# Performance work log

Measured on AMD Instinct MI355X. Metric: run time of the kernel, lower is better.

## Reference

```python
import jax, jax.numpy as jnp
import numpy as np

TEMPERATURE = 2.0
SOFT_LAMBDA = 0.5
SMOOTH_L1_BETA = 1.0  # CFG.smooth_l1_beta (torch default)
EPS_COS = 1e-8
EPS_LOG = 1e-7


def _offdiag(x):
    # x: [n, n] -> [n, n-1], dropping the diagonal, preserving column order.
    n = x.shape[0]
    cols = jnp.arange(n - 1)
    idx = cols[None, :] + (cols[None, :] >= jnp.arange(n)[:, None])
    return x[jnp.arange(n)[:, None], idx]


def _cos_pair_diff(v):
    # 1 - pairwise cosine similarity, norms clamped at eps (torch CosineSimilarity).
    nv = jnp.maximum(jnp.linalg.norm(v, axis=-1), EPS_COS)
    cos = (v @ v.T) / (nv[:, None] * nv[None, :])
    return 1.0 - cos


def setup_inputs() -> dict:
    key = jax.random.key(0)
    k1, k2, k3, k4, k5 = jax.random.split(key, 5)
    n, d_feat = 384, 128
    return {
        "trans_feat": jax.random.normal(k1, (n, d_feat), dtype=jnp.float32),
        "rot_green": jax.random.normal(k2, (n, 3), dtype=jnp.float32),
        "rot_red": jax.random.normal(k3, (n, 3), dtype=jnp.float32),
        "trans": jax.random.normal(k4, (n, 3), dtype=jnp.float32),
        "sym": jax.random.randint(k5, (n, 1), 0, 2, dtype=jnp.int32),
    }


def reference(trans_feat, rot_green, rot_red, trans, sym):
    n = trans_feat.shape[0]

    # ---- label differences ----
    # trans: smooth-L1 over pairwise diffs, mean over coord dim -> [n, n]
    d = trans[:, None, :] - trans[None, :, :]
    ad = jnp.abs(d)
    sl1 = jnp.where(ad < SMOOTH_L1_BETA, 0.5 * d * d / SMOOTH_L1_BETA, ad - 0.5 * SMOOTH_L1_BETA)
    trans_diff = sl1.mean(-1)

    g = _cos_pair_diff(rot_green)
    r = _cos_pair_diff(rot_red)
    sym_mask = sym[:, 0] == 1
    pair_sym = sym_mask[:, None] | sym_mask[None, :]
    rot_diff = jnp.where(pair_sym, g, g + r)

    # ---- feature similarity logits (negative L2, zero-safe norm) ----
    fd = trans_feat[:, None, :] - trans_feat[None, :, :]
    sq = jnp.sum(fd * fd, axis=-1)
    norm = jnp.where(sq > 0, jnp.sqrt(jnp.where(sq > 0, sq, 1.0)), 0.0)
    logits = -norm / TEMPERATURE
    logits = logits - jnp.max(logits, axis=1, keepdims=True)
    exp_logits = jnp.exp(logits)

    lo = _offdiag(logits)      # [n, n-1]
    eo = _offdiag(exp_logits)  # [n, n-1]
    td = _offdiag(trans_diff)  # [n, n-1]
    rd = _offdiag(rot_diff)    # [n, n-1]

    # rank masks: mask[i, j, k] = diff[i, j] <= diff[i, k]
    trans_mask = td[:, :, None] <= td[:, None, :]
    hard_mask = trans_mask & (rd[:, :, None] <= rd[:, None, :])

    den_trans = jnp.einsum('ijk,ik->ij', trans_mask.astype(lo.dtype), eo)
    den_hard = jnp.einsum('ijk,ik->ij', hard_mask.astype(lo.dtype), eo)

    pos_trans = lo - jnp.log(den_trans + EPS_LOG)
    pos_hard = lo - jnp.log(den_hard + EPS_LOG)

    denom = n * (n - 1)
    loss_hard = -jnp.sum(pos_hard) / denom
    loss_trans = -jnp.sum(pos_trans) / denom
    return loss_hard + SOFT_LAMBDA * loss_trans
```

## Files before the change

kernel.cpp:

```cpp
#include <hip/hip_runtime.h>
#include <math.h>

#define N 384
#define HB 192
#define DF 128
#define TEMP 2.0f
#define SOFT_LAMBDA 0.5f
#define BETA 1.0f
#define EPS_COS 1e-8f
#define EPS_LOG 1e-7f

__global__ __launch_bounds__(192) void rnc_main(
    const float* __restrict__ feat,
    const float* __restrict__ rg,
    const float* __restrict__ rr,
    const float* __restrict__ tr,
    const int*   __restrict__ sym,
    float* __restrict__ partial_h,
    float* __restrict__ partial_t)
{
    const int i = blockIdx.x >> 1;
    const int h = blockIdx.x & 1;
    const int t = threadIdx.x;

    __shared__ __align__(16) float4 pk[N];
    __shared__ __align__(16) float2 dp[HB][4];
    __shared__ __align__(16) float fi[DF];
    __shared__ float hdr[12];
    __shared__ float red_h[3], red_t[3];

    if (t < DF) fi[t] = feat[i * DF + t];
    if (t == 0) {
        hdr[0] = tr[i * 3 + 0];
        hdr[1] = tr[i * 3 + 1];
        hdr[2] = tr[i * 3 + 2];
        float g0 = rg[i * 3 + 0], g1 = rg[i * 3 + 1], g2 = rg[i * 3 + 2];
        hdr[3] = g0; hdr[4] = g1; hdr[5] = g2;
        hdr[6] = fmaxf(sqrtf(g0 * g0 + g1 * g1 + g2 * g2), EPS_COS);
        float r0 = rr[i * 3 + 0], r1 = rr[i * 3 + 1], r2 = rr[i * 3 + 2];
        hdr[7] = r0; hdr[8] = r1; hdr[9] = r2;
        hdr[10] = fmaxf(sqrtf(r0 * r0 + r1 * r1 + r2 * r2), EPS_COS);
        hdr[11] = (sym[i] == 1) ? 1.0f : 0.0f;
    }
    __syncthreads();

    for (int e = t; e < N; e += HB) {
        const float4* fj4 = reinterpret_cast<const float4*>(feat + e * DF);
        const float4* fi4 = reinterpret_cast<const float4*>(fi);
        float sq = 0.f;
#pragma unroll 8
        for (int d = 0; d < DF / 4; ++d) {
            float4 a = fi4[d];
            float4 b = fj4[d];
            float dx = a.x - b.x, dy = a.y - b.y, dz = a.z - b.z, dw = a.w - b.w;
            sq += dx * dx + dy * dy + dz * dz + dw * dw;
        }
        float dist = (sq > 0.f) ? sqrtf(sq) : 0.f;
        float lo = -dist * (1.0f / TEMP);
        float eo = (e == i) ? 0.f : expf(lo);

        float s = 0.f;
#pragma unroll
        for (int c = 0; c < 3; ++c) {
            float d_ = hdr[c] - tr[e * 3 + c];
            float ad = fabsf(d_);
            s += (ad < BETA) ? (0.5f * d_ * d_ / BETA) : (ad - 0.5f * BETA);
        }
        float td = s * (1.0f / 3.0f);

        float g0 = rg[e * 3 + 0], g1 = rg[e * 3 + 1], g2 = rg[e * 3 + 2];
        float ng = fmaxf(sqrtf(g0 * g0 + g1 * g1 + g2 * g2), EPS_COS);
        float gdiff = 1.0f - (hdr[3] * g0 + hdr[4] * g1 + hdr[5] * g2) / (hdr[6] * ng);
        float r0 = rr[e * 3 + 0], r1 = rr[e * 3 + 1], r2 = rr[e * 3 + 2];
        float nr = fmaxf(sqrtf(r0 * r0 + r1 * r1 + r2 * r2), EPS_COS);
        float rdiff = 1.0f - (hdr[7] * r0 + hdr[8] * r1 + hdr[9] * r2) / (hdr[10] * nr);
        bool pair_sym = (hdr[11] != 0.0f) || (sym[e] == 1);
        float rd = pair_sym ? gdiff : (gdiff + rdiff);

        pk[e] = make_float4(td, rd, eo, lo);
    }
    __syncthreads();

    const int kg = t >> 6;
    const int l  = t & 63;
    const int jl = l * 3;
    float tdj[3], rdj[3];
    float dent[3] = {0.f, 0.f, 0.f};
    float denh[3] = {0.f, 0.f, 0.f};
#pragma unroll
    for (int jj = 0; jj < 3; ++jj) {
        float4 p = pk[h * HB + jl + jj];
        tdj[jj] = p.x;
        rdj[jj] = p.y;
    }
    const int k0 = kg * (N / 3);
#pragma unroll 4
    for (int k = k0; k < k0 + N / 3; ++k) {
        float4 p = pk[k];
#pragma unroll
        for (int jj = 0; jj < 3; ++jj) {
            bool mt = p.x >= tdj[jj];
            bool mh = mt && (p.y >= rdj[jj]);
            dent[jj] += mt ? p.z : 0.f;
            denh[jj] += mh ? p.z : 0.f;
        }
    }
#pragma unroll
    for (int jj = 0; jj < 3; ++jj) dp[jl + jj][kg] = make_float2(dent[jj], denh[jj]);
    __syncthreads();

    float st_ = 0.f, sh_ = 0.f;
#pragma unroll
    for (int g = 0; g < 3; ++g) {
        float2 v = dp[t][g];
        st_ += v.x;
        sh_ += v.y;
    }
    const int j = h * HB + t;
    float pos_h = 0.f, pos_t = 0.f;
    if (j != i) {
        float lo = pk[j].w;
        pos_h = lo - logf(sh_ + EPS_LOG);
        pos_t = lo - logf(st_ + EPS_LOG);
    }
#pragma unroll
    for (int off = 32; off > 0; off >>= 1) {
        pos_h += __shfl_down(pos_h, off, 64);
        pos_t += __shfl_down(pos_t, off, 64);
    }
    if (l == 0) {
        red_h[kg] = pos_h;
        red_t[kg] = pos_t;
    }
    __syncthreads();
    if (t == 0) {
        partial_h[blockIdx.x] = red_h[0] + red_h[1] + red_h[2];
        partial_t[blockIdx.x] = red_t[0] + red_t[1] + red_t[2];
    }
}

__global__ __launch_bounds__(768) void rnc_final(
    const float* __restrict__ partial_h,
    const float* __restrict__ partial_t,
    float* __restrict__ out)
{
    const int t = threadIdx.x;
    float hsum = partial_h[t];
    float tsum = partial_t[t];
#pragma unroll
    for (int off = 32; off > 0; off >>= 1) {
        hsum += __shfl_down(hsum, off, 64);
        tsum += __shfl_down(tsum, off, 64);
    }
    __shared__ float rh[12], rt[12];
    const int wave = t >> 6, lane = t & 63;
    if (lane == 0) {
        rh[wave] = hsum;
        rt[wave] = tsum;
    }
    __syncthreads();
    if (t == 0) {
        double sh = 0.0, st = 0.0;
#pragma unroll
        for (int w = 0; w < 12; ++w) {
            sh += (double)rh[w];
            st += (double)rt[w];
        }
        const double denom = (double)N * (double)(N - 1);
        out[0] = (float)(-(sh + (double)SOFT_LAMBDA * st) / denom);
    }
}

extern "C" void kernel_launch(void* const* d_in, const int* in_sizes, int n_in,
                              void* d_out, int out_size, void* d_ws, size_t ws_size,
                              hipStream_t stream) {
    const float* feat = (const float*)d_in[0];
    const float* rg   = (const float*)d_in[1];
    const float* rr   = (const float*)d_in[2];
    const float* tr   = (const float*)d_in[3];
    const int*   sym  = (const int*)d_in[4];
    float* out = (float*)d_out;

    float* partial_h = (float*)d_ws;
    float* partial_t = partial_h + 2 * N;

    rnc_main<<<2 * N, HB, 0, stream>>>(feat, rg, rr, tr, sym, partial_h, partial_t);
    rnc_final<<<1, 2 * N, 0, stream>>>(partial_h, partial_t, out);
}
```

Before: 93.45 us.

## Split pairwise feature computation into tiled kernel and widen rank kernel

Moves the pairwise distance, label-difference and exp computation into a separate 16x16-tiled kernel that stages both feature rows in shared memory and writes a full N×N float4 pair table to workspace. The rank kernel then loads one row of that table and uses 512 threads (8 k-groups) instead of 192, which shortens each thread's comparison loop. The aim is to avoid having every block re-read 384 feature rows from global memory, and to give the quadratic rank loop more parallelism. In exchange it adds an extra kernel launch, a 2.3 MB write and read-back of the pair table, and needs a larger workspace.

```diff
diff --git a/kernel.cpp b/kernel.cpp
--- a/kernel.cpp
+++ b/kernel.cpp
@@ -2,20 +2,98 @@
 #include <math.h>
 
 #define N 384
-#define HB 192
 #define DF 128
+#define TI 16
+#define TK 16
 #define TEMP 2.0f
 #define SOFT_LAMBDA 0.5f
 #define BETA 1.0f
 #define EPS_COS 1e-8f
 #define EPS_LOG 1e-7f
 
-__global__ __launch_bounds__(192) void rnc_main(
+__global__ __launch_bounds__(256) void rnc_pairs(
     const float* __restrict__ feat,
     const float* __restrict__ rg,
     const float* __restrict__ rr,
     const float* __restrict__ tr,
     const int*   __restrict__ sym,
+    float4* __restrict__ pk)
+{
+    const int i0 = blockIdx.y * TI;
+    const int k0 = blockIdx.x * TK;
+    const int t = threadIdx.x;
+
+    __shared__ __align__(16) float4 fi_s[TI][DF / 4 + 1];
+    __shared__ __align__(16) float4 fk_s[TK][DF / 4 + 1];
+    __shared__ float4 hi_s[TI], gi_s[TI], ri_s[TI];
+    __shared__ float4 hk_s[TK], gk_s[TK], rk_s[TK];
+
+    if (t < TI) {
+        int g = i0 + t;
+        hi_s[t] = make_float4(tr[g * 3], tr[g * 3 + 1], tr[g * 3 + 2],
+                              (sym[g] == 1) ? 1.f : 0.f);
+        float a = rg[g * 3], b = rg[g * 3 + 1], c = rg[g * 3 + 2];
+        gi_s[t] = make_float4(a, b, c, fmaxf(sqrtf(a * a + b * b + c * c), EPS_COS));
+        float d = rr[g * 3], e = rr[g * 3 + 1], f = rr[g * 3 + 2];
+        ri_s[t] = make_float4(d, e, f, fmaxf(sqrtf(d * d + e * e + f * f), EPS_COS));
+    } else if (t >= 32 && t < 32 + TK) {
+        int g = k0 + (t - 32);
+        int tl = t - 32;
+        hk_s[tl] = make_float4(tr[g * 3], tr[g * 3 + 1], tr[g * 3 + 2],
+                               (sym[g] == 1) ? 1.f : 0.f);
+        float a = rg[g * 3], b = rg[g * 3 + 1], c = rg[g * 3 + 2];
+        gk_s[tl] = make_float4(a, b, c, fmaxf(sqrtf(a * a + b * b + c * c), EPS_COS));
+        float d = rr[g * 3], e = rr[g * 3 + 1], f = rr[g * 3 + 2];
+        rk_s[tl] = make_float4(d, e, f, fmaxf(sqrtf(d * d + e * e + f * f), EPS_COS));
+    }
+
+    const float4* feat4 = reinterpret_cast<const float4*>(feat);
+#pragma unroll
+    for (int idx = 0; idx < 2; ++idx) {
+        int u = t + idx * 256;
+        int row = u >> 5, c = u & 31;
+        fi_s[row][c] = feat4[(i0 + row) * (DF / 4) + c];
+        fk_s[row][c] = feat4[(k0 + row) * (DF / 4) + c];
+    }
+    __syncthreads();
+
+    const int ii = t >> 4, kk = t & 15;
+    float sq = 0.f;
+#pragma unroll
+    for (int d = 0; d < DF / 4; ++d) {
+        float4 a = fi_s[ii][d];
+        float4 b = fk_s[kk][d];
+        float dx = a.x - b.x, dy = a.y - b.y, dz = a.z - b.z, dw = a.w - b.w;
+        sq += dx * dx + dy * dy + dz * dz + dw * dw;
+    }
+    const int gi = i0 + ii, gk = k0 + kk;
+    float dist = (sq > 0.f) ? sqrtf(sq) : 0.f;
+    float lo = -dist * (1.0f / TEMP);
+    float eo = (gi == gk) ? 0.f : expf(lo);
+
+    float4 ha = hi_s[ii], hb = hk_s[kk];
+    float s = 0.f;
+    {
+        float d0 = ha.x - hb.x, d1 = ha.y - hb.y, d2 = ha.z - hb.z;
+        float a0 = fabsf(d0), a1 = fabsf(d1), a2 = fabsf(d2);
+        s += (a0 < BETA) ? (0.5f * d0 * d0 / BETA) : (a0 - 0.5f * BETA);
+        s += (a1 < BETA) ? (0.5f * d1 * d1 / BETA) : (a1 - 0.5f * BETA);
+        s += (a2 < BETA) ? (0.5f * d2 * d2 / BETA) : (a2 - 0.5f * BETA);
+    }
+    float td = s * (1.0f / 3.0f);
+
+    float4 ga = gi_s[ii], gb = gk_s[kk];
+    float gdiff = 1.0f - (ga.x * gb.x + ga.y * gb.y + ga.z * gb.z) / (ga.w * gb.w);
+    float4 ra = ri_s[ii], rb = rk_s[kk];
+    float rdiff = 1.0f - (ra.x * rb.x + ra.y * rb.y + ra.z * rb.z) / (ra.w * rb.w);
+    bool pair_sym = (ha.w != 0.f) || (hb.w != 0.f);
+    float rd = pair_sym ? gdiff : (gdiff + rdiff);
+
+    pk[gi * N + gk] = make_float4(td, rd, eo, lo);
+}
+
+__global__ __launch_bounds__(512) void rnc_rank(
+    const float4* __restrict__ pk,
     float* __restrict__ partial_h,
     float* __restrict__ partial_t)
 {
@@ -23,80 +101,28 @@
     const int h = blockIdx.x & 1;
     const int t = threadIdx.x;
 
-    __shared__ __align__(16) float4 pk[N];
-    __shared__ __align__(16) float2 dp[HB][4];
-    __shared__ __align__(16) float fi[DF];
-    __shared__ float hdr[12];
-    __shared__ float red_h[3], red_t[3];
-
-    if (t < DF) fi[t] = feat[i * DF + t];
-    if (t == 0) {
-        hdr[0] = tr[i * 3 + 0];
-        hdr[1] = tr[i * 3 + 1];
-        hdr[2] = tr[i * 3 + 2];
-        float g0 = rg[i * 3 + 0], g1 = rg[i * 3 + 1], g2 = rg[i * 3 + 2];
-        hdr[3] = g0; hdr[4] = g1; hdr[5] = g2;
-        hdr[6] = fmaxf(sqrtf(g0 * g0 + g1 * g1 + g2 * g2), EPS_COS);
-        float r0 = rr[i * 3 + 0], r1 = rr[i * 3 + 1], r2 = rr[i * 3 + 2];
-        hdr[7] = r0; hdr[8] = r1; hdr[9] = r2;
-        hdr[10] = fmaxf(sqrtf(r0 * r0 + r1 * r1 + r2 * r2), EPS_COS);
-        hdr[11] = (sym[i] == 1) ? 1.0f : 0.0f;
-    }
-    __syncthreads();
-
-    for (int e = t; e < N; e += HB) {
-        const float4* fj4 = reinterpret_cast<const float4*>(feat + e * DF);
-        const float4* fi4 = reinterpret_cast<const float4*>(fi);
-        float sq = 0.f;
-#pragma unroll 8
-        for (int d = 0; d < DF / 4; ++d) {
-            float4 a = fi4[d];
-            float4 b = fj4[d];
-            float dx = a.x - b.x, dy = a.y - b.y, dz = a.z - b.z, dw = a.w - b.w;
-            sq += dx * dx + dy * dy + dz * dz + dw * dw;
-        }
-        float dist = (sq > 0.f) ? sqrtf(sq) : 0.f;
-        float lo = -dist * (1.0f / TEMP);
-        float eo = (e == i) ? 0.f : expf(lo);
-
-        float s = 0.f;
-#pragma unroll
-        for (int c = 0; c < 3; ++c) {
-            float d_ = hdr[c] - tr[e * 3 + c];
-            float ad = fabsf(d_);
-            s += (ad < BETA) ? (0.5f * d_ * d_ / BETA) : (ad - 0.5f * BETA);
-        }
-        float td = s * (1.0f / 3.0f);
-
-        float g0 = rg[e * 3 + 0], g1 = rg[e * 3 + 1], g2 = rg[e * 3 + 2];
-        float ng = fmaxf(sqrtf(g0 * g0 + g1 * g1 + g2 * g2), EPS_COS);
-        float gdiff = 1.0f - (hdr[3] * g0 + hdr[4] * g1 + hdr[5] * g2) / (hdr[6] * ng);
-        float r0 = rr[e * 3 + 0], r1 = rr[e * 3 + 1], r2 = rr[e * 3 + 2];
-        float nr = fmaxf(sqrtf(r0 * r0 + r1 * r1 + r2 * r2), EPS_COS);
-        float rdiff = 1.0f - (hdr[7] * r0 + hdr[8] * r1 + hdr[9] * r2) / (hdr[10] * nr);
-        bool pair_sym = (hdr[11] != 0.0f) || (sym[e] == 1);
-        float rd = pair_sym ? gdiff : (gdiff + rdiff);
-
-        pk[e] = make_float4(td, rd, eo, lo);
-    }
-    __syncthreads();
-
-    const int kg = t >> 6;
-    const int l  = t & 63;
+    __shared__ __align__(16) float4 pks[N];
+    __shared__ __align__(16) float2 dp[192][8];
+    __shared__ float red_h[8], red_t[8];
+
+    if (t < N) pks[t] = pk[i * N + t];
+    __syncthreads();
+
+    const int w = t >> 6, l = t & 63;
     const int jl = l * 3;
     float tdj[3], rdj[3];
     float dent[3] = {0.f, 0.f, 0.f};
     float denh[3] = {0.f, 0.f, 0.f};
 #pragma unroll
     for (int jj = 0; jj < 3; ++jj) {
-        float4 p = pk[h * HB + jl + jj];
+        float4 p = pks[h * 192 + jl + jj];
         tdj[jj] = p.x;
         rdj[jj] = p.y;
     }
-    const int k0 = kg * (N / 3);
+    const int k0 = w * 48;
 #pragma unroll 4
-    for (int k = k0; k < k0 + N / 3; ++k) {
-        float4 p = pk[k];
+    for (int k = k0; k < k0 + 48; ++k) {
+        float4 p = pks[k];
 #pragma unroll
         for (int jj = 0; jj < 3; ++jj) {
             bool mt = p.x >= tdj[jj];
@@ -106,22 +132,24 @@
         }
     }
 #pragma unroll
-    for (int jj = 0; jj < 3; ++jj) dp[jl + jj][kg] = make_float2(dent[jj], denh[jj]);
-    __syncthreads();
-
-    float st_ = 0.f, sh_ = 0.f;
-#pragma unroll
-    for (int g = 0; g < 3; ++g) {
-        float2 v = dp[t][g];
-        st_ += v.x;
-        sh_ += v.y;
-    }
-    const int j = h * HB + t;
+    for (int jj = 0; jj < 3; ++jj) dp[jl + jj][w] = make_float2(dent[jj], denh[jj]);
+    __syncthreads();
+
     float pos_h = 0.f, pos_t = 0.f;
-    if (j != i) {
-        float lo = pk[j].w;
-        pos_h = lo - logf(sh_ + EPS_LOG);
-        pos_t = lo - logf(st_ + EPS_LOG);
+    if (t < 192) {
+        const int j = h * 192 + t;
+        if (j != i) {
+            float st_ = 0.f, sh_ = 0.f;
+#pragma unroll
+            for (int g = 0; g < 8; ++g) {
+                float2 v = dp[t][g];
+                st_ += v.x;
+                sh_ += v.y;
+            }
+            float lo = pks[j].w;
+            pos_h = lo - logf(sh_ + EPS_LOG);
+            pos_t = lo - logf(st_ + EPS_LOG);
+        }
     }
 #pragma unroll
     for (int off = 32; off > 0; off >>= 1) {
@@ -129,13 +157,19 @@
         pos_t += __shfl_down(pos_t, off, 64);
     }
     if (l == 0) {
-        red_h[kg] = pos_h;
-        red_t[kg] = pos_t;
+        red_h[w] = pos_h;
+        red_t[w] = pos_t;
     }
     __syncthreads();
     if (t == 0) {
-        partial_h[blockIdx.x] = red_h[0] + red_h[1] + red_h[2];
-        partial_t[blockIdx.x] = red_t[0] + red_t[1] + red_t[2];
+        float sh = 0.f, st = 0.f;
+#pragma unroll
+        for (int g = 0; g < 8; ++g) {
+            sh += red_h[g];
+            st += red_t[g];
+        }
+        partial_h[blockIdx.x] = sh;
+        partial_t[blockIdx.x] = st;
     }
 }
 
@@ -181,9 +215,12 @@
     const int*   sym  = (const int*)d_in[4];
     float* out = (float*)d_out;
 
-    float* partial_h = (float*)d_ws;
+    float4* pk = (float4*)d_ws;
+    float* partial_h = (float*)((char*)d_ws + (size_t)N * N * sizeof(float4));
     float* partial_t = partial_h + 2 * N;
 
-    rnc_main<<<2 * N, HB, 0, stream>>>(feat, rg, rr, tr, sym, partial_h, partial_t);
+    dim3 gridA(N / TK, N / TI);
+    rnc_pairs<<<gridA, 256, 0, stream>>>(feat, rg, rr, tr, sym, pk);
+    rnc_rank<<<2 * N, 512, 0, stream>>>(pk, partial_h, partial_t);
     rnc_final<<<1, 2 * N, 0, stream>>>(partial_h, partial_t, out);
 }
```

New measurement: 79.81 us. 1.17x faster.
